# Kernel tuning notes

Hardware: AMD Instinct MI355X
Metric: run time of the kernel (lower is better)

The kernel has to match this reference:

```python
import jax, jax.numpy as jnp
import numpy as np

D = 3072      # hidden_dim == flattened CIFAR image size
KF = 1        # FourierFeature k (default, KAN_FourierAttention does not pass k)
NP = 5        # module-level n -> size of w and n parameter vectors
NC = 100      # num_classes
B = 512


def setup_inputs() -> dict:
    key = jax.random.key(0)
    ks = jax.random.split(key, 7)
    return {
        "x": jax.random.normal(ks[0], (B, 3, 32, 32), dtype=jnp.float32),
        "a": jax.random.normal(ks[1], (D, D, KF), dtype=jnp.float32),
        "b": jax.random.normal(ks[2], (D, D, KF), dtype=jnp.float32),
        "w": jax.random.normal(ks[3], (NP,), dtype=jnp.float32),
        "n_param": jax.random.normal(ks[4], (NP,), dtype=jnp.float32),
        "fc_w": jax.random.normal(ks[5], (NC, D), dtype=jnp.float32) * 0.02,
        "fc_b": jax.random.normal(ks[6], (NC,), dtype=jnp.float32) * 0.02,
    }


def reference(x, a, b, w, n_param, fc_w, fc_b):
    xf = x.reshape(x.shape[0], -1)                 # [B, D]
    m = jnp.arange(1, KF + 1, dtype=xf.dtype)      # [KF]
    cos_part = jnp.cos(xf[..., None] * m)          # [B, D, KF]
    sin_part = jnp.sin(xf[..., None] * m)          # [B, D, KF]
    # Original: result[b,i,j] = sum_k cos[b,j,k]*a[i,j,k] + sin[b,j,k]*b[i,j,k]
    # then part2[b,j] = sum_i result[b,i,j].  Fuse both reductions (over i and k)
    # to avoid materializing the [B, D, D, KF] broadcast intermediate.
    part2 = (jnp.einsum('bdk,idk->bd', cos_part, a)
             + jnp.einsum('bdk,idk->bd', sin_part, b))   # [B, D]
    # part1: scalar accumulated over i=1..len(n)-1
    part1 = jnp.sum(w[1:] * n_param[1:] + w[:-1] * n_param[:-1])
    Z = part1 + part2                               # [B, D]
    return Z @ fc_w.T + fc_b                        # [B, NC]
```

## Files before the change

kernel.cpp:

```cpp
#include <hip/hip_runtime.h>
#include <math.h>

#define D 3072
#define BATCH 512
#define NCLS 100
#define KS 32
#define KCHUNK (D / KS)

typedef __attribute__((ext_vector_type(8))) short bf16x8;
typedef __attribute__((ext_vector_type(4))) float f32x4;

#define WS_OFF_W   24576
#define WS_OFF_P   712704
#define WS_NEED    (WS_OFF_P + (size_t)KS * BATCH * NCLS * 4)

__device__ inline unsigned short f2bf(float f) {
    unsigned u = __float_as_uint(f);
    u += 0x7FFF + ((u >> 16) & 1);
    return (unsigned short)(u >> 16);
}

__global__ __launch_bounds__(256) void prep_kernel(const float* __restrict__ a,
                                                   const float* __restrict__ b,
                                                   const float* __restrict__ fcw,
                                                   float* __restrict__ ws,
                                                   unsigned short* __restrict__ Wb) {
    const int bid = blockIdx.x;
    const int t   = threadIdx.x;
    if (bid < 288) {
        const int rc   = bid / 3;
        const int cg   = bid % 3;
        const int col  = cg * 1024 + t * 4;
        const int row0 = rc * 32;
        float4 sa = make_float4(0.f, 0.f, 0.f, 0.f);
        float4 sb = make_float4(0.f, 0.f, 0.f, 0.f);
        #pragma unroll
        for (int r = 0; r < 32; ++r) {
            const int i = row0 + r;
            const float4 va = *(const float4*)(a + i * D + col);
            const float4 vb = *(const float4*)(b + i * D + col);
            sa.x += va.x; sa.y += va.y; sa.z += va.z; sa.w += va.w;
            sb.x += vb.x; sb.y += vb.y; sb.z += vb.z; sb.w += vb.w;
        }
        atomicAdd(&ws[col + 0], sa.x);
        atomicAdd(&ws[col + 1], sa.y);
        atomicAdd(&ws[col + 2], sa.z);
        atomicAdd(&ws[col + 3], sa.w);
        atomicAdd(&ws[D + col + 0], sb.x);
        atomicAdd(&ws[D + col + 1], sb.y);
        atomicAdd(&ws[D + col + 2], sb.z);
        atomicAdd(&ws[D + col + 3], sb.w);
    } else {
        const int idx = (bid - 288) * 256 + t;
        const int c   = idx / (D / 4);
        const int d   = (idx % (D / 4)) * 4;
        ushort4 o;
        if (c < NCLS) {
            const float4 v = *(const float4*)(fcw + c * D + d);
            o.x = f2bf(v.x); o.y = f2bf(v.y); o.z = f2bf(v.z); o.w = f2bf(v.w);
        } else {
            o.x = o.y = o.z = o.w = 0;
        }
        *(ushort4*)(Wb + c * D + d) = o;
    }
}

__global__ __launch_bounds__(256) void fzgemm_kernel(
        const float* __restrict__ x,
        const float* __restrict__ w5,
        const float* __restrict__ n5,
        const float* __restrict__ ws,
        const unsigned short* __restrict__ Wb,
        float* __restrict__ part) {
    const int wave = threadIdx.x >> 6;
    const int lane = threadIdx.x & 63;
    const int l16  = lane & 15;
    const int quad = lane >> 4;
    const int m0   = blockIdx.x * 64 + wave * 16;
    const int j    = blockIdx.y;
    const int kb   = j * KCHUNK + quad * 8;

    float part1 = 0.f;
    #pragma unroll
    for (int i = 0; i < 4; ++i)
        part1 += w5[i + 1] * n5[i + 1] + w5[i] * n5[i];

    f32x4 acc[7];
    #pragma unroll
    for (int n = 0; n < 7; ++n) acc[n] = (f32x4){0.f, 0.f, 0.f, 0.f};

    const float* xr = x + (m0 + l16) * D;

    #pragma unroll
    for (int kk = 0; kk < KCHUNK; kk += 32) {
        const int col = kb + kk;
        const float4 xv0 = *(const float4*)(xr + col);
        const float4 xv1 = *(const float4*)(xr + col + 4);
        const float4 Av0 = *(const float4*)(ws + col);
        const float4 Av1 = *(const float4*)(ws + col + 4);
        const float4 Bv0 = *(const float4*)(ws + D + col);
        const float4 Bv1 = *(const float4*)(ws + D + col + 4);

        union { bf16x8 v; unsigned short s[8]; } af;
        float sv, cv;
        __sincosf(xv0.x, &sv, &cv); af.s[0] = f2bf(part1 + cv * Av0.x + sv * Bv0.x);
        __sincosf(xv0.y, &sv, &cv); af.s[1] = f2bf(part1 + cv * Av0.y + sv * Bv0.y);
        __sincosf(xv0.z, &sv, &cv); af.s[2] = f2bf(part1 + cv * Av0.z + sv * Bv0.z);
        __sincosf(xv0.w, &sv, &cv); af.s[3] = f2bf(part1 + cv * Av0.w + sv * Bv0.w);
        __sincosf(xv1.x, &sv, &cv); af.s[4] = f2bf(part1 + cv * Av1.x + sv * Bv1.x);
        __sincosf(xv1.y, &sv, &cv); af.s[5] = f2bf(part1 + cv * Av1.y + sv * Bv1.y);
        __sincosf(xv1.z, &sv, &cv); af.s[6] = f2bf(part1 + cv * Av1.z + sv * Bv1.z);
        __sincosf(xv1.w, &sv, &cv); af.s[7] = f2bf(part1 + cv * Av1.w + sv * Bv1.w);

        #pragma unroll
        for (int n = 0; n < 7; ++n) {
            const bf16x8 bf = *(const bf16x8*)(Wb + (n * 16 + l16) * D + col);
            acc[n] = __builtin_amdgcn_mfma_f32_16x16x32_bf16(af.v, bf, acc[n], 0, 0, 0);
        }
    }

    float* pb = part + (size_t)j * (BATCH * NCLS);
    #pragma unroll
    for (int n = 0; n < 7; ++n) {
        const int c = n * 16 + l16;
        if (c < NCLS) {
            #pragma unroll
            for (int r = 0; r < 4; ++r)
                pb[(m0 + quad * 4 + r) * NCLS + c] = acc[n][r];
        }
    }
}

__global__ __launch_bounds__(256) void reduce2_kernel(const float* __restrict__ part,
                                                      const float* __restrict__ fcb,
                                                      float* __restrict__ out) {
    const int idx = blockIdx.x * 256 + threadIdx.x;
    if (idx >= BATCH * NCLS) return;
    const int c = idx % NCLS;
    float s = fcb[c];
    #pragma unroll
    for (int ks = 0; ks < KS; ++ks)
        s += part[ks * (BATCH * NCLS) + idx];
    out[idx] = s;
}

__global__ __launch_bounds__(256) void fused_gemm_kernel(
        const float* __restrict__ x,
        const float* __restrict__ w5,
        const float* __restrict__ n5,
        const float* __restrict__ fcw,
        const float* __restrict__ fcb,
        const float* __restrict__ ws,
        float* __restrict__ out) {
    __shared__ __align__(16) float Zl[32 * 36];
    __shared__ __align__(16) float Wl[32 * 132];
    const int t  = threadIdx.x;
    const int bt = blockIdx.x;
    const int j  = blockIdx.y;
    float part1 = 0.f;
    #pragma unroll
    for (int i = 0; i < 4; ++i)
        part1 += w5[i + 1] * n5[i + 1] + w5[i] * n5[i];
    const int c0 = (t & 31) * 4;
    const int b0 = (t >> 5) * 4;
    const int kl = t & 31;
    const int tg = t >> 5;
    const int bbase = bt * 32;
    float acc[4][4];
    #pragma unroll
    for (int i = 0; i < 4; ++i)
        #pragma unroll
        for (int q = 0; q < 4; ++q) acc[i][q] = 0.f;
    for (int s = 0; s < 3; ++s) {
        const int dbase = j * 96 + s * 32;
        for (int idx = t; idx < NCLS * 32; idx += 256) {
            const int c = idx >> 5;
            const int k = idx & 31;
            Wl[k * 132 + c] = fcw[c * D + dbase + k];
        }
        const float Av = ws[dbase + kl];
        const float Bv = ws[D + dbase + kl];
        #pragma unroll
        for (int i = 0; i < 4; ++i) {
            const int bl = tg + i * 8;
            const float xv = x[(bbase + bl) * D + dbase + kl];
            float sv, cv;
            sincosf(xv, &sv, &cv);
            Zl[bl * 36 + kl] = part1 + cv * Av + sv * Bv;
        }
        __syncthreads();
        #pragma unroll
        for (int k = 0; k < 32; ++k) {
            const float4 wv = *(const float4*)&Wl[k * 132 + c0];
            float zb[4];
            #pragma unroll
            for (int bj = 0; bj < 4; ++bj) zb[bj] = Zl[(b0 + bj) * 36 + k];
            #pragma unroll
            for (int bj = 0; bj < 4; ++bj) {
                acc[bj][0] += zb[bj] * wv.x;
                acc[bj][1] += zb[bj] * wv.y;
                acc[bj][2] += zb[bj] * wv.z;
                acc[bj][3] += zb[bj] * wv.w;
            }
        }
        __syncthreads();
    }
    if (c0 < NCLS) {
        #pragma unroll
        for (int bj = 0; bj < 4; ++bj) {
            const int row = bbase + b0 + bj;
            #pragma unroll
            for (int q = 0; q < 4; ++q) {
                const int c = c0 + q;
                if (c < NCLS) {
                    float v = acc[bj][q];
                    if (j == 0) v += fcb[c];
                    atomicAdd(&out[row * NCLS + c], v);
                }
            }
        }
    }
}

extern "C" void kernel_launch(void* const* d_in, const int* in_sizes, int n_in,
                              void* d_out, int out_size, void* d_ws, size_t ws_size,
                              hipStream_t stream) {
    const float* x   = (const float*)d_in[0];
    const float* a   = (const float*)d_in[1];
    const float* b   = (const float*)d_in[2];
    const float* w5  = (const float*)d_in[3];
    const float* n5  = (const float*)d_in[4];
    const float* fcw = (const float*)d_in[5];
    const float* fcb = (const float*)d_in[6];
    float* out = (float*)d_out;
    float* wsf = (float*)d_ws;

    hipMemsetAsync(d_ws, 0, 2 * D * sizeof(float), stream);

    if (ws_size >= WS_NEED) {
        unsigned short* Wb = (unsigned short*)((char*)d_ws + WS_OFF_W);
        float*          Pp = (float*)((char*)d_ws + WS_OFF_P);
        prep_kernel<<<dim3(624), 256, 0, stream>>>(a, b, fcw, wsf, Wb);
        fzgemm_kernel<<<dim3(8, KS), 256, 0, stream>>>(x, w5, n5, wsf, Wb, Pp);
        reduce2_kernel<<<dim3(200), 256, 0, stream>>>(Pp, fcb, out);
    } else {
        hipMemsetAsync(d_out, 0, (size_t)out_size * sizeof(float), stream);
        prep_kernel<<<dim3(288), 256, 0, stream>>>(a, b, fcw, wsf,
                                                   (unsigned short*)d_ws );
        fused_gemm_kernel<<<dim3(16, 32), 256, 0, stream>>>(x, w5, n5, fcw, fcb,
                                                            wsf, out);
    }
}
```

Measured before the change: 128.2 us.

## Replace colsum atomics with partial sums, store bf16 split-K partials

The prep kernel now writes per-row-chunk partial column sums of a and b to the workspace instead of atomically adding into a zeroed buffer, which removes the memset and the atomic contention. The GEMM kernel finishes the 96-way reduction for its K-chunk into shared memory before the main loop. Split-K partials are stored as bf16 and the final reduce reads packed pairs, halving the partial traffic. The cost is extra redundant reads of the partial sums across the M blocks, plus lower precision in the partial accumulation.

```diff
diff --git a/kernel.cpp b/kernel.cpp
--- a/kernel.cpp
+++ b/kernel.cpp
@@ -6,24 +6,28 @@
 #define NCLS 100
 #define KS 32
 #define KCHUNK (D / KS)
+#define RC 96
 
 typedef __attribute__((ext_vector_type(8))) short bf16x8;
 typedef __attribute__((ext_vector_type(4))) float f32x4;
 
-#define WS_OFF_W   24576
-#define WS_OFF_P   712704
-#define WS_NEED    (WS_OFF_P + (size_t)KS * BATCH * NCLS * 4)
+#define WS_OFF_W   2359296
+#define WS_OFF_P   3047424
+#define WS_NEED    (WS_OFF_P + (size_t)KS * BATCH * NCLS * 2)
 
 __device__ inline unsigned short f2bf(float f) {
     unsigned u = __float_as_uint(f);
     u += 0x7FFF + ((u >> 16) & 1);
     return (unsigned short)(u >> 16);
 }
+__device__ inline float bf2f(unsigned short s) {
+    return __uint_as_float(((unsigned)s) << 16);
+}
 
 __global__ __launch_bounds__(256) void prep_kernel(const float* __restrict__ a,
                                                    const float* __restrict__ b,
                                                    const float* __restrict__ fcw,
-                                                   float* __restrict__ ws,
+                                                   float* __restrict__ pws,
                                                    unsigned short* __restrict__ Wb) {
     const int bid = blockIdx.x;
     const int t   = threadIdx.x;
@@ -42,14 +46,8 @@
             sa.x += va.x; sa.y += va.y; sa.z += va.z; sa.w += va.w;
             sb.x += vb.x; sb.y += vb.y; sb.z += vb.z; sb.w += vb.w;
         }
-        atomicAdd(&ws[col + 0], sa.x);
-        atomicAdd(&ws[col + 1], sa.y);
-        atomicAdd(&ws[col + 2], sa.z);
-        atomicAdd(&ws[col + 3], sa.w);
-        atomicAdd(&ws[D + col + 0], sb.x);
-        atomicAdd(&ws[D + col + 1], sb.y);
-        atomicAdd(&ws[D + col + 2], sb.z);
-        atomicAdd(&ws[D + col + 3], sb.w);
+        *(float4*)(pws + rc * D + col)            = sa;
+        *(float4*)(pws + (RC + rc) * D + col)     = sb;
     } else {
         const int idx = (bid - 288) * 256 + t;
         const int c   = idx / (D / 4);
@@ -69,16 +67,35 @@
         const float* __restrict__ x,
         const float* __restrict__ w5,
         const float* __restrict__ n5,
-        const float* __restrict__ ws,
+        const float* __restrict__ pws,
         const unsigned short* __restrict__ Wb,
-        float* __restrict__ part) {
-    const int wave = threadIdx.x >> 6;
-    const int lane = threadIdx.x & 63;
+        unsigned short* __restrict__ part) {
+    __shared__ float Al[KCHUNK];
+    __shared__ float Bl[KCHUNK];
+
+    const int t    = threadIdx.x;
+    const int wave = t >> 6;
+    const int lane = t & 63;
     const int l16  = lane & 15;
     const int quad = lane >> 4;
     const int m0   = blockIdx.x * 64 + wave * 16;
     const int j    = blockIdx.y;
-    const int kb   = j * KCHUNK + quad * 8;
+    const int cbase = j * KCHUNK;
+
+    if (t < KCHUNK) {
+        float s = 0.f;
+        #pragma unroll 8
+        for (int rc = 0; rc < RC; ++rc)
+            s += pws[rc * D + cbase + t];
+        Al[t] = s;
+    } else if (t >= 128 && t < 128 + KCHUNK) {
+        const int c = t - 128;
+        float s = 0.f;
+        #pragma unroll 8
+        for (int rc = 0; rc < RC; ++rc)
+            s += pws[(RC + rc) * D + cbase + c];
+        Bl[c] = s;
+    }
 
     float part1 = 0.f;
     #pragma unroll
@@ -90,16 +107,18 @@
     for (int n = 0; n < 7; ++n) acc[n] = (f32x4){0.f, 0.f, 0.f, 0.f};
 
     const float* xr = x + (m0 + l16) * D;
+    __syncthreads();
 
     #pragma unroll
     for (int kk = 0; kk < KCHUNK; kk += 32) {
-        const int col = kb + kk;
-        const float4 xv0 = *(const float4*)(xr + col);
-        const float4 xv1 = *(const float4*)(xr + col + 4);
-        const float4 Av0 = *(const float4*)(ws + col);
-        const float4 Av1 = *(const float4*)(ws + col + 4);
-        const float4 Bv0 = *(const float4*)(ws + D + col);
-        const float4 Bv1 = *(const float4*)(ws + D + col + 4);
+        const int lcol = quad * 8 + kk;
+        const int gcol = cbase + lcol;
+        const float4 xv0 = *(const float4*)(xr + gcol);
+        const float4 xv1 = *(const float4*)(xr + gcol + 4);
+        const float4 Av0 = *(const float4*)&Al[lcol];
+        const float4 Av1 = *(const float4*)&Al[lcol + 4];
+        const float4 Bv0 = *(const float4*)&Bl[lcol];
+        const float4 Bv1 = *(const float4*)&Bl[lcol + 4];
 
         union { bf16x8 v; unsigned short s[8]; } af;
         float sv, cv;
@@ -114,34 +133,58 @@
 
         #pragma unroll
         for (int n = 0; n < 7; ++n) {
-            const bf16x8 bf = *(const bf16x8*)(Wb + (n * 16 + l16) * D + col);
+            const bf16x8 bf = *(const bf16x8*)(Wb + (n * 16 + l16) * D + gcol);
             acc[n] = __builtin_amdgcn_mfma_f32_16x16x32_bf16(af.v, bf, acc[n], 0, 0, 0);
         }
     }
 
-    float* pb = part + (size_t)j * (BATCH * NCLS);
+    unsigned short* pb = part + (size_t)j * (BATCH * NCLS);
     #pragma unroll
     for (int n = 0; n < 7; ++n) {
         const int c = n * 16 + l16;
         if (c < NCLS) {
             #pragma unroll
             for (int r = 0; r < 4; ++r)
-                pb[(m0 + quad * 4 + r) * NCLS + c] = acc[n][r];
-        }
-    }
-}
-
-__global__ __launch_bounds__(256) void reduce2_kernel(const float* __restrict__ part,
-                                                      const float* __restrict__ fcb,
-                                                      float* __restrict__ out) {
+                pb[(m0 + quad * 4 + r) * NCLS + c] = f2bf(acc[n][r]);
+        }
+    }
+}
+
+__global__ __launch_bounds__(256) void reduce2_kernel(
+        const unsigned int* __restrict__ partu,
+        const float* __restrict__ fcb,
+        float* __restrict__ out) {
     const int idx = blockIdx.x * 256 + threadIdx.x;
-    if (idx >= BATCH * NCLS) return;
-    const int c = idx % NCLS;
-    float s = fcb[c];
-    #pragma unroll
-    for (int ks = 0; ks < KS; ++ks)
-        s += part[ks * (BATCH * NCLS) + idx];
-    out[idx] = s;
+    const int c   = (idx * 2) % NCLS;
+    float s0 = fcb[c];
+    float s1 = fcb[c + 1];
+    #pragma unroll
+    for (int ks = 0; ks < KS; ++ks) {
+        const unsigned int v = partu[ks * (BATCH * NCLS / 2) + idx];
+        s0 += bf2f((unsigned short)(v & 0xFFFF));
+        s1 += bf2f((unsigned short)(v >> 16));
+    }
+    *(float2*)(out + idx * 2) = make_float2(s0, s1);
+}
+
+__global__ __launch_bounds__(256) void colsum_atomic_kernel(
+        const float* __restrict__ a, const float* __restrict__ b,
+        float* __restrict__ ws) {
+    const int col  = (blockIdx.x % 3) * 1024 + threadIdx.x * 4;
+    const int row0 = (blockIdx.x / 3) * 32;
+    float4 sa = make_float4(0.f, 0.f, 0.f, 0.f);
+    float4 sb = make_float4(0.f, 0.f, 0.f, 0.f);
+    #pragma unroll
+    for (int r = 0; r < 32; ++r) {
+        const float4 va = *(const float4*)(a + (row0 + r) * D + col);
+        const float4 vb = *(const float4*)(b + (row0 + r) * D + col);
+        sa.x += va.x; sa.y += va.y; sa.z += va.z; sa.w += va.w;
+        sb.x += vb.x; sb.y += vb.y; sb.z += vb.z; sb.w += vb.w;
+    }
+    atomicAdd(&ws[col + 0], sa.x); atomicAdd(&ws[col + 1], sa.y);
+    atomicAdd(&ws[col + 2], sa.z); atomicAdd(&ws[col + 3], sa.w);
+    atomicAdd(&ws[D + col + 0], sb.x); atomicAdd(&ws[D + col + 1], sb.y);
+    atomicAdd(&ws[D + col + 2], sb.z); atomicAdd(&ws[D + col + 3], sb.w);
 }
 
 __global__ __launch_bounds__(256) void fused_gemm_kernel(
@@ -235,18 +278,17 @@
     float* out = (float*)d_out;
     float* wsf = (float*)d_ws;
 
-    hipMemsetAsync(d_ws, 0, 2 * D * sizeof(float), stream);
-
     if (ws_size >= WS_NEED) {
         unsigned short* Wb = (unsigned short*)((char*)d_ws + WS_OFF_W);
-        float*          Pp = (float*)((char*)d_ws + WS_OFF_P);
+        unsigned short* Pp = (unsigned short*)((char*)d_ws + WS_OFF_P);
         prep_kernel<<<dim3(624), 256, 0, stream>>>(a, b, fcw, wsf, Wb);
         fzgemm_kernel<<<dim3(8, KS), 256, 0, stream>>>(x, w5, n5, wsf, Wb, Pp);
-        reduce2_kernel<<<dim3(200), 256, 0, stream>>>(Pp, fcb, out);
+        reduce2_kernel<<<dim3(100), 256, 0, stream>>>((const unsigned int*)Pp,
+                                                      fcb, out);
     } else {
+        hipMemsetAsync(d_ws, 0, 2 * D * sizeof(float), stream);
         hipMemsetAsync(d_out, 0, (size_t)out_size * sizeof(float), stream);
-        prep_kernel<<<dim3(288), 256, 0, stream>>>(a, b, fcw, wsf,
-                                                   (unsigned short*)d_ws );
+        colsum_atomic_kernel<<<dim3(288), 256, 0, stream>>>(a, b, wsf);
         fused_gemm_kernel<<<dim3(16, 32), 256, 0, stream>>>(x, w5, n5, fcw, fcb,
                                                             wsf, out);
     }
```

After: 126.3 us. About the same (-1.4%).
